# Kernel tuning notes

Measured on AMD Instinct MI355X. Metric: run time of the kernel, lower is better.

## Reference

```python
import jax, jax.numpy as jnp
import numpy as np

D_MODEL = 1024
NUM_HEADS = 16
HEAD_DIM = D_MODEL // NUM_HEADS
NEG = -1e9


def setup_inputs() -> dict:
    key = jax.random.key(0)
    kx, kq, kk, kv, ko = jax.random.split(key, 5)
    scale = 1.0 / np.sqrt(D_MODEL)
    x = jax.random.normal(kx, (4, 2048, D_MODEL), dtype=jnp.float32)
    Wq = jax.random.normal(kq, (D_MODEL, D_MODEL), dtype=jnp.float32) * scale
    Wk = jax.random.normal(kk, (D_MODEL, D_MODEL), dtype=jnp.float32) * scale
    Wv = jax.random.normal(kv, (D_MODEL, D_MODEL), dtype=jnp.float32) * scale
    Wo = jax.random.normal(ko, (D_MODEL, D_MODEL), dtype=jnp.float32) * scale
    return {"x": x, "Wq": Wq, "Wk": Wk, "Wv": Wv, "Wo": Wo}


def reference(x, Wq, Wk, Wv, Wo):
    B, S, _ = x.shape
    # torch Linear: y = x @ W.T
    q = (x @ Wq.T).reshape(B, S, NUM_HEADS, HEAD_DIM).transpose(0, 2, 1, 3)
    k = (x @ Wk.T).reshape(B, S, NUM_HEADS, HEAD_DIM).transpose(0, 2, 1, 3)
    v = (x @ Wv.T).reshape(B, S, NUM_HEADS, HEAD_DIM).transpose(0, 2, 1, 3)
    scores = jnp.einsum("bhqd,bhkd->bhqk", q, k) / jnp.sqrt(jnp.float32(HEAD_DIM))
    # additive causal mask: strictly-upper-triangular entries get -1e9 (as in source)
    mask = jnp.triu(jnp.ones((S, S), dtype=scores.dtype), k=1) * NEG
    scores = scores + mask
    attn = jax.nn.softmax(scores, axis=-1)  # dropout p=0.0 -> identity
    out = jnp.einsum("bhqk,bhkd->bhqd", attn, v)
    out = out.transpose(0, 2, 1, 3).reshape(B, S, D_MODEL)
    return out @ Wo.T
```

## Files before the change

kernel.cpp:

```cpp
#include <hip/hip_runtime.h>

typedef __attribute__((ext_vector_type(8))) short short8;
typedef __attribute__((ext_vector_type(4))) short short4v;
typedef __attribute__((ext_vector_type(4))) float f32x4;
typedef __attribute__((ext_vector_type(4))) unsigned int u32x4;

static __device__ __forceinline__ unsigned short f2bf(float f){
  unsigned u = __builtin_bit_cast(unsigned, f);
  unsigned r = u + 0x7fffu + ((u >> 16) & 1u);
  return (unsigned short)(r >> 16);
}

static __device__ __forceinline__ float exp2_fast(float x){
  float r; asm("v_exp_f32 %0, %1" : "=v"(r) : "v"(x)); return r;
}

static __device__ __forceinline__ void g2lds16(const unsigned short* g, unsigned short* l){
  __builtin_amdgcn_global_load_lds(
      (const __attribute__((address_space(1))) void*)g,
      (__attribute__((address_space(3))) void*)l, 16, 0, 0);
}

__global__ __launch_bounds__(256) void cast_bf16_kernel(const float* __restrict__ in,
                                                        unsigned short* __restrict__ out, int n8){
  int i = blockIdx.x * 256 + threadIdx.x;
  if (i >= n8) return;
  const float4* p = (const float4*)in + (size_t)i * 2;
  float4 a = p[0], b = p[1];
  short8 o;
  o[0] = (short)f2bf(a.x); o[1] = (short)f2bf(a.y); o[2] = (short)f2bf(a.z); o[3] = (short)f2bf(a.w);
  o[4] = (short)f2bf(b.x); o[5] = (short)f2bf(b.y); o[6] = (short)f2bf(b.z); o[7] = (short)f2bf(b.w);
  *(short8*)(out + (size_t)i * 8) = o;
}

__global__ __launch_bounds__(256) void cast_w4_kernel(const float* __restrict__ w0,
                                                      const float* __restrict__ w1,
                                                      const float* __restrict__ w2,
                                                      const float* __restrict__ w3,
                                                      unsigned short* __restrict__ o0,
                                                      unsigned short* __restrict__ o1,
                                                      unsigned short* __restrict__ o2,
                                                      unsigned short* __restrict__ o3){
  const int z = blockIdx.y;
  const float* in = (z == 0) ? w0 : (z == 1) ? w1 : (z == 2) ? w2 : w3;
  unsigned short* out = (z == 0) ? o0 : (z == 1) ? o1 : (z == 2) ? o2 : o3;
  int i = blockIdx.x * 256 + threadIdx.x;
  const float4* p = (const float4*)in + (size_t)i * 2;
  float4 a = p[0], b = p[1];
  short8 o;
  o[0] = (short)f2bf(a.x); o[1] = (short)f2bf(a.y); o[2] = (short)f2bf(a.z); o[3] = (short)f2bf(a.w);
  o[4] = (short)f2bf(b.x); o[5] = (short)f2bf(b.y); o[6] = (short)f2bf(b.z); o[7] = (short)f2bf(b.w);
  *(short8*)(out + (size_t)i * 8) = o;
}

template<int MODE>
__global__ __launch_bounds__(256) void gemm_nt(
    const unsigned short* __restrict__ A,
    const unsigned short* __restrict__ B0, const unsigned short* __restrict__ B1,
    const unsigned short* __restrict__ B2,
    unsigned short* __restrict__ q0, unsigned short* __restrict__ q1, unsigned short* __restrict__ q2,
    float* __restrict__ fout,
    int M, int N, int K)
{
  __shared__ unsigned short As[128 * 32];
  __shared__ unsigned short Bs[128 * 32];
  const int z = blockIdx.y;
  const unsigned short* __restrict__ B = (z == 0) ? B0 : ((z == 1) ? B1 : B2);
  unsigned short* __restrict__ qo = (z == 0) ? q0 : ((z == 1) ? q1 : q2);
  const int ntn = N >> 7;
  const int nwg = gridDim.x, cpx = nwg >> 3;
  const int bid = blockIdx.x;
  const int swz = (bid & 7) * cpx + (bid >> 3);
  const int tm = swz / ntn, tn = swz % ntn;
  const int m0 = tm << 7, n0 = tn << 7;
  const int t = threadIdx.x;
  const int w = t >> 6;
  const int l = t & 63, lo = l & 15, hi = l >> 4;
  const int wr = w >> 1, wc = w & 1;
  f32x4 acc[4][4];
#pragma unroll
  for (int i = 0; i < 4; ++i)
#pragma unroll
    for (int j = 0; j < 4; ++j) acc[i][j] = (f32x4){0.f, 0.f, 0.f, 0.f};

  const int arow0 = t >> 2, cg = t & 3;
  for (int kk = 0; kk < K; kk += 32){
#pragma unroll
    for (int r = 0; r < 2; ++r){
      int row = r * 64 + arow0;
      g2lds16(&A[(size_t)(m0 + row) * K + kk + cg * 8], &As[r * 2048 + w * 512]);
      g2lds16(&B[(size_t)(n0 + row) * K + kk + cg * 8], &Bs[r * 2048 + w * 512]);
    }
    __syncthreads();
    short8 af[4], bf[4];
#pragma unroll
    for (int mi = 0; mi < 4; ++mi) af[mi] = *(const short8*)&As[(wr * 64 + mi * 16 + lo) * 32 + hi * 8];
#pragma unroll
    for (int ni = 0; ni < 4; ++ni) bf[ni] = *(const short8*)&Bs[(wc * 64 + ni * 16 + lo) * 32 + hi * 8];
#pragma unroll
    for (int mi = 0; mi < 4; ++mi)
#pragma unroll
      for (int ni = 0; ni < 4; ++ni)
        acc[mi][ni] = __builtin_amdgcn_mfma_f32_16x16x32_bf16(af[mi], bf[ni], acc[mi][ni], 0, 0, 0);
    __syncthreads();
  }
#pragma unroll
  for (int mi = 0; mi < 4; ++mi){
#pragma unroll
    for (int ni = 0; ni < 4; ++ni){
#pragma unroll
      for (int j = 0; j < 4; ++j){
        int m = m0 + wr * 64 + mi * 16 + hi * 4 + j;
        int n = n0 + wc * 64 + ni * 16 + lo;
        float v = acc[mi][ni][j];
        if (MODE == 0){
          int b = m >> 11, s = m & 2047, h = n >> 6, d = n & 63;
          qo[((((size_t)b * 16 + h) * 2048 + s) << 6) + d] = f2bf(v);
        } else {
          fout[(size_t)m * N + n] = v;
        }
      }
    }
  }
}

__global__ __launch_bounds__(256) void transpose_v(const unsigned short* __restrict__ V,
                                                   unsigned short* __restrict__ Vt){
  __shared__ unsigned short tile[64 * 72];
  const int bh = blockIdx.y;
  const int s0 = blockIdx.x << 6;
  const int t = threadIdx.x;
  const size_t base = (size_t)bh * 2048 * 64;
#pragma unroll
  for (int r = 0; r < 2; ++r){
    int c = r * 256 + t;
    int sr = c >> 3, cgp = c & 7;
    *(short8*)&tile[sr * 72 + cgp * 8] = *(const short8*)&V[base + (size_t)(s0 + sr) * 64 + cgp * 8];
  }
  __syncthreads();
  const int d = t >> 2, sc = t & 3;
  unsigned short vals[16];
#pragma unroll
  for (int i = 0; i < 16; ++i) vals[i] = tile[(sc * 16 + i) * 72 + d];
  unsigned short* op = Vt + base + (size_t)d * 2048 + s0 + sc * 16;
  *(short8*)op = *(const short8*)&vals[0];
  *(short8*)(op + 8) = *(const short8*)&vals[8];
}

__global__ __launch_bounds__(256) void attn_kernel(
    const unsigned short* __restrict__ Q, const unsigned short* __restrict__ K,
    const unsigned short* __restrict__ Vt, unsigned short* __restrict__ O)
{
  __shared__ unsigned short Klds[2][64 * 64];
  __shared__ unsigned short Vlds[2][64 * 64];
  const int bid = blockIdx.x;
  const int xcd = bid & 7, rank = bid >> 3;
  const int bh = xcd * 8 + (rank >> 4);
  const int p = rank & 15;
  const int t = threadIdx.x, w = t >> 6, l = t & 63, lo = l & 15, hi = l >> 4;
  const size_t bb = (size_t)bh * 2048 * 64;
  const int bat = bh >> 4, h = bh & 15;
  const int srow0 = w * 8 + (l >> 3);
  const int su0 = l & 7;
  const float cexp = 0.125f * 1.44269504f;

#define STAGE(bufi, kv0) do { \
  _Pragma("unroll") \
  for (int i_ = 0; i_ < 2; ++i_){ \
    int row_ = i_ * 32 + srow0; \
    int us_ = su0 ^ (row_ & 7); \
    g2lds16(&K[bb + (size_t)((kv0) + row_) * 64 + us_ * 8], &Klds[bufi][i_ * 2048 + w * 512]); \
    g2lds16(&Vt[bb + (size_t)row_ * 2048 + (kv0) + us_ * 8], &Vlds[bufi][i_ * 2048 + w * 512]); \
  } \
} while (0)

#pragma unroll 1
  for (int ph = 0; ph < 2; ++ph){
    const int qt = ph ? (31 - p) : p;
    const int qr = qt * 64 + w * 16;
    short8 aq[2];
#pragma unroll
    for (int kg = 0; kg < 2; ++kg)
      aq[kg] = *(const short8*)&Q[bb + (size_t)(qr + lo) * 64 + kg * 32 + hi * 8];
    f32x4 accO[4];
#pragma unroll
    for (int i = 0; i < 4; ++i) accO[i] = (f32x4){0.f, 0.f, 0.f, 0.f};
    float m2 = -3e38f, lsum = 0.f;

    STAGE(0, 0);
    __syncthreads();
    int buf = 0;

#pragma unroll 1
    for (int s = 0; s <= qt; ++s){
      if (s < qt) STAGE(buf ^ 1, (s + 1) * 64);
      const unsigned short* Kl = &Klds[buf][0];
      const unsigned short* Vl = &Vlds[buf][0];
      f32x4 sa[4];
#pragma unroll
      for (int i = 0; i < 4; ++i) sa[i] = (f32x4){0.f, 0.f, 0.f, 0.f};
      __builtin_amdgcn_s_setprio(1);
#pragma unroll
      for (int ni = 0; ni < 4; ++ni)
#pragma unroll
        for (int kg = 0; kg < 2; ++kg){
          int u = (kg * 4 + hi) ^ (lo & 7);
          short8 kf = *(const short8*)&Kl[(ni * 16 + lo) * 64 + u * 8];
          sa[ni] = __builtin_amdgcn_mfma_f32_16x16x32_bf16(kf, aq[kg], sa[ni], 0, 0, 0);
        }
      __builtin_amdgcn_s_setprio(0);
      if (s == qt){
        const int qg = qr + lo;
        const int kv0 = s * 64;
#pragma unroll
        for (int ni = 0; ni < 4; ++ni)
#pragma unroll
          for (int j = 0; j < 4; ++j){
            int kv = kv0 + ni * 16 + hi * 4 + j;
            if (kv > qg) sa[ni][j] = -1e9f;
          }
      }
      float pm = fmaxf(fmaxf(sa[0][0], sa[0][1]), fmaxf(sa[0][2], sa[0][3]));
      pm = fmaxf(pm, fmaxf(fmaxf(sa[1][0], sa[1][1]), fmaxf(sa[1][2], sa[1][3])));
      pm = fmaxf(pm, fmaxf(fmaxf(sa[2][0], sa[2][1]), fmaxf(sa[2][2], sa[2][3])));
      pm = fmaxf(pm, fmaxf(fmaxf(sa[3][0], sa[3][1]), fmaxf(sa[3][2], sa[3][3])));
      float pms = pm * cexp;
      if (!__all(pms <= m2 + 8.0f)){
        float pr = fmaxf(pms, __shfl_xor(pms, 16, 64));
        pr = fmaxf(pr, __shfl_xor(pr, 32, 64));
        float m2n = fmaxf(m2, pr);
        float corr = exp2_fast(m2 - m2n);
        m2 = m2n;
        lsum *= corr;
        float cj[4];
#pragma unroll
        for (int j = 0; j < 4; ++j) cj[j] = __shfl(corr, hi * 4 + j, 64);
#pragma unroll
        for (int dt = 0; dt < 4; ++dt)
#pragma unroll
          for (int j = 0; j < 4; ++j) accO[dt][j] *= cj[j];
      }
      float rs = 0.f;
#pragma unroll
      for (int ni = 0; ni < 4; ++ni)
#pragma unroll
        for (int j = 0; j < 4; ++j){
          float pv = exp2_fast(fmaf(sa[ni][j], cexp, -m2));
          sa[ni][j] = pv;
          rs += pv;
        }
      rs += __shfl_xor(rs, 16, 64);
      rs += __shfl_xor(rs, 32, 64);
      lsum += rs;
      short8 pa[2];
#pragma unroll
      for (int kg = 0; kg < 2; ++kg){
        unsigned r0, r1, r2, r3;
        asm("v_cvt_pk_bf16_f32 %0, %1, %2" : "=v"(r0) : "v"(sa[2*kg][0]),   "v"(sa[2*kg][1]));
        asm("v_cvt_pk_bf16_f32 %0, %1, %2" : "=v"(r1) : "v"(sa[2*kg][2]),   "v"(sa[2*kg][3]));
        asm("v_cvt_pk_bf16_f32 %0, %1, %2" : "=v"(r2) : "v"(sa[2*kg+1][0]), "v"(sa[2*kg+1][1]));
        asm("v_cvt_pk_bf16_f32 %0, %1, %2" : "=v"(r3) : "v"(sa[2*kg+1][2]), "v"(sa[2*kg+1][3]));
        u32x4 pk; pk[0] = r0; pk[1] = r1; pk[2] = r2; pk[3] = r3;
        pa[kg] = __builtin_bit_cast(short8, pk);
      }
      __builtin_amdgcn_s_setprio(1);
#pragma unroll
      for (int dt = 0; dt < 4; ++dt)
#pragma unroll
        for (int kg = 0; kg < 2; ++kg){
          short4v c0, c1;
          {
            int u = ((kg * 2 + 0) * 2 + (hi >> 1)) ^ (lo & 7);
            c0 = *(const short4v*)&Vl[(dt * 16 + lo) * 64 + u * 8 + (hi & 1) * 4];
          }
          {
            int u = ((kg * 2 + 1) * 2 + (hi >> 1)) ^ (lo & 7);
            c1 = *(const short4v*)&Vl[(dt * 16 + lo) * 64 + u * 8 + (hi & 1) * 4];
          }
          short8 vb = (short8){c0[0], c0[1], c0[2], c0[3], c1[0], c1[1], c1[2], c1[3]};
          accO[dt] = __builtin_amdgcn_mfma_f32_16x16x32_bf16(pa[kg], vb, accO[dt], 0, 0, 0);
        }
      __builtin_amdgcn_s_setprio(0);
      __syncthreads();
      buf ^= 1;
    }
    float lr = 1.0f / lsum;
    float lj[4];
#pragma unroll
    for (int j = 0; j < 4; ++j) lj[j] = __shfl(lr, hi * 4 + j, 64);
#pragma unroll
    for (int dt = 0; dt < 4; ++dt)
#pragma unroll
      for (int j = 0; j < 4; ++j){
        int srow = qr + hi * 4 + j;
        O[((size_t)(bat * 2048 + srow) << 10) + h * 64 + dt * 16 + lo] = f2bf(accO[dt][j] * lj[j]);
      }
  }
#undef STAGE
}

extern "C" void kernel_launch(void* const* d_in, const int* in_sizes, int n_in,
                              void* d_out, int out_size, void* d_ws, size_t ws_size,
                              hipStream_t stream){
  (void)in_sizes; (void)n_in; (void)out_size; (void)ws_size;
  const float* x  = (const float*)d_in[0];
  const float* Wq = (const float*)d_in[1];
  const float* Wk = (const float*)d_in[2];
  const float* Wv = (const float*)d_in[3];
  const float* Wo = (const float*)d_in[4];
  char* ws = (char*)d_ws;
  const size_t MB = 1024 * 1024;
  unsigned short* XB  = (unsigned short*)(ws);
  unsigned short* WQB = (unsigned short*)(ws + 16 * MB);
  unsigned short* WKB = (unsigned short*)(ws + 18 * MB);
  unsigned short* WVB = (unsigned short*)(ws + 20 * MB);
  unsigned short* WOB = (unsigned short*)(ws + 22 * MB);
  unsigned short* Qb  = (unsigned short*)(ws + 24 * MB);
  unsigned short* Kb  = (unsigned short*)(ws + 40 * MB);
  unsigned short* Vb  = (unsigned short*)(ws + 56 * MB);
  unsigned short* Vtb = (unsigned short*)(ws + 72 * MB);
  unsigned short* Ob  = XB;

  cast_bf16_kernel<<<dim3(4096), 256, 0, stream>>>(x, XB, 8388608 / 8);
  cast_w4_kernel<<<dim3(512, 4), 256, 0, stream>>>(Wq, Wk, Wv, Wo, WQB, WKB, WVB, WOB);

  gemm_nt<0><<<dim3(512, 3), 256, 0, stream>>>(XB, WQB, WKB, WVB, Qb, Kb, Vb, nullptr,
                                               8192, 1024, 1024);
  transpose_v<<<dim3(32, 64), 256, 0, stream>>>(Vb, Vtb);
  attn_kernel<<<dim3(1024), 256, 0, stream>>>(Qb, Kb, Vtb, Ob);
  gemm_nt<1><<<dim3(512, 1), 256, 0, stream>>>(Ob, WOB, WOB, WOB, nullptr, nullptr, nullptr,
                                               (float*)d_out, 8192, 1024, 1024);
}
```

Baseline: 199.7 us.

## Split paired causal q-tiles into separate blocks and drop LDS double buffering

Each attention block now handles a single 64-row query tile instead of a balanced pair, with twice as many blocks launched and the heaviest tiles scheduled first. The K/V LDS staging is reduced to a single buffer, loaded synchronously each iteration. This halves LDS use to raise occupancy and finer-grained load balance, at the cost of losing the overlap between next-tile loads and current-tile compute.

```diff
diff --git a/kernel.cpp b/kernel.cpp
--- a/kernel.cpp
+++ b/kernel.cpp
@@ -151,12 +151,12 @@
     const unsigned short* __restrict__ Q, const unsigned short* __restrict__ K,
     const unsigned short* __restrict__ Vt, unsigned short* __restrict__ O)
 {
-  __shared__ unsigned short Klds[2][64 * 64];
-  __shared__ unsigned short Vlds[2][64 * 64];
+  __shared__ unsigned short Klds[64 * 64];
+  __shared__ unsigned short Vlds[64 * 64];
   const int bid = blockIdx.x;
   const int xcd = bid & 7, rank = bid >> 3;
-  const int bh = xcd * 8 + (rank >> 4);
-  const int p = rank & 15;
+  const int bh = xcd * 8 + (rank >> 5);
+  const int qt = 31 - (rank & 31);
   const int t = threadIdx.x, w = t >> 6, l = t & 63, lo = l & 15, hi = l >> 4;
   const size_t bb = (size_t)bh * 2048 * 64;
   const int bat = bh >> 4, h = bh & 15;
@@ -164,139 +164,126 @@
   const int su0 = l & 7;
   const float cexp = 0.125f * 1.44269504f;
 
-#define STAGE(bufi, kv0) do { \
-  _Pragma("unroll") \
-  for (int i_ = 0; i_ < 2; ++i_){ \
-    int row_ = i_ * 32 + srow0; \
-    int us_ = su0 ^ (row_ & 7); \
-    g2lds16(&K[bb + (size_t)((kv0) + row_) * 64 + us_ * 8], &Klds[bufi][i_ * 2048 + w * 512]); \
-    g2lds16(&Vt[bb + (size_t)row_ * 2048 + (kv0) + us_ * 8], &Vlds[bufi][i_ * 2048 + w * 512]); \
-  } \
-} while (0)
+  const int qr = qt * 64 + w * 16;
+  short8 aq[2];
+#pragma unroll
+  for (int kg = 0; kg < 2; ++kg)
+    aq[kg] = *(const short8*)&Q[bb + (size_t)(qr + lo) * 64 + kg * 32 + hi * 8];
+  f32x4 accO[4];
+#pragma unroll
+  for (int i = 0; i < 4; ++i) accO[i] = (f32x4){0.f, 0.f, 0.f, 0.f};
+  float m2 = -3e38f, lsum = 0.f;
 
 #pragma unroll 1
-  for (int ph = 0; ph < 2; ++ph){
-    const int qt = ph ? (31 - p) : p;
-    const int qr = qt * 64 + w * 16;
-    short8 aq[2];
-#pragma unroll
-    for (int kg = 0; kg < 2; ++kg)
-      aq[kg] = *(const short8*)&Q[bb + (size_t)(qr + lo) * 64 + kg * 32 + hi * 8];
-    f32x4 accO[4];
-#pragma unroll
-    for (int i = 0; i < 4; ++i) accO[i] = (f32x4){0.f, 0.f, 0.f, 0.f};
-    float m2 = -3e38f, lsum = 0.f;
-
-    STAGE(0, 0);
+  for (int s = 0; s <= qt; ++s){
+    const int kv0 = s * 64;
+#pragma unroll
+    for (int i_ = 0; i_ < 2; ++i_){
+      int row_ = i_ * 32 + srow0;
+      int us_ = su0 ^ (row_ & 7);
+      g2lds16(&K[bb + (size_t)(kv0 + row_) * 64 + us_ * 8], &Klds[i_ * 2048 + w * 512]);
+      g2lds16(&Vt[bb + (size_t)row_ * 2048 + kv0 + us_ * 8], &Vlds[i_ * 2048 + w * 512]);
+    }
     __syncthreads();
-    int buf = 0;
-
-#pragma unroll 1
-    for (int s = 0; s <= qt; ++s){
-      if (s < qt) STAGE(buf ^ 1, (s + 1) * 64);
-      const unsigned short* Kl = &Klds[buf][0];
-      const unsigned short* Vl = &Vlds[buf][0];
-      f32x4 sa[4];
-#pragma unroll
-      for (int i = 0; i < 4; ++i) sa[i] = (f32x4){0.f, 0.f, 0.f, 0.f};
-      __builtin_amdgcn_s_setprio(1);
+    const unsigned short* Kl = &Klds[0];
+    const unsigned short* Vl = &Vlds[0];
+    f32x4 sa[4];
+#pragma unroll
+    for (int i = 0; i < 4; ++i) sa[i] = (f32x4){0.f, 0.f, 0.f, 0.f};
+    __builtin_amdgcn_s_setprio(1);
+#pragma unroll
+    for (int ni = 0; ni < 4; ++ni)
+#pragma unroll
+      for (int kg = 0; kg < 2; ++kg){
+        int u = (kg * 4 + hi) ^ (lo & 7);
+        short8 kf = *(const short8*)&Kl[(ni * 16 + lo) * 64 + u * 8];
+        sa[ni] = __builtin_amdgcn_mfma_f32_16x16x32_bf16(kf, aq[kg], sa[ni], 0, 0, 0);
+      }
+    __builtin_amdgcn_s_setprio(0);
+    if (s == qt){
+      const int qg = qr + lo;
 #pragma unroll
       for (int ni = 0; ni < 4; ++ni)
 #pragma unroll
-        for (int kg = 0; kg < 2; ++kg){
-          int u = (kg * 4 + hi) ^ (lo & 7);
-          short8 kf = *(const short8*)&Kl[(ni * 16 + lo) * 64 + u * 8];
-          sa[ni] = __builtin_amdgcn_mfma_f32_16x16x32_bf16(kf, aq[kg], sa[ni], 0, 0, 0);
+        for (int j = 0; j < 4; ++j){
+          int kv = kv0 + ni * 16 + hi * 4 + j;
+          if (kv > qg) sa[ni][j] = -1e9f;
         }
-      __builtin_amdgcn_s_setprio(0);
-      if (s == qt){
-        const int qg = qr + lo;
-        const int kv0 = s * 64;
-#pragma unroll
-        for (int ni = 0; ni < 4; ++ni)
-#pragma unroll
-          for (int j = 0; j < 4; ++j){
-            int kv = kv0 + ni * 16 + hi * 4 + j;
-            if (kv > qg) sa[ni][j] = -1e9f;
-          }
+    }
+    float pm = fmaxf(fmaxf(sa[0][0], sa[0][1]), fmaxf(sa[0][2], sa[0][3]));
+    pm = fmaxf(pm, fmaxf(fmaxf(sa[1][0], sa[1][1]), fmaxf(sa[1][2], sa[1][3])));
+    pm = fmaxf(pm, fmaxf(fmaxf(sa[2][0], sa[2][1]), fmaxf(sa[2][2], sa[2][3])));
+    pm = fmaxf(pm, fmaxf(fmaxf(sa[3][0], sa[3][1]), fmaxf(sa[3][2], sa[3][3])));
+    float pms = pm * cexp;
+    if (!__all(pms <= m2 + 8.0f)){
+      float pr = fmaxf(pms, __shfl_xor(pms, 16, 64));
+      pr = fmaxf(pr, __shfl_xor(pr, 32, 64));
+      float m2n = fmaxf(m2, pr);
+      float corr = exp2_fast(m2 - m2n);
+      m2 = m2n;
+      lsum *= corr;
+      float cj[4];
+#pragma unroll
+      for (int j = 0; j < 4; ++j) cj[j] = __shfl(corr, hi * 4 + j, 64);
+#pragma unroll
+      for (int dt = 0; dt < 4; ++dt)
+#pragma unroll
+        for (int j = 0; j < 4; ++j) accO[dt][j] *= cj[j];
+    }
+    float rs = 0.f;
+#pragma unroll
+    for (int ni = 0; ni < 4; ++ni)
+#pragma unroll
+      for (int j = 0; j < 4; ++j){
+        float pv = exp2_fast(fmaf(sa[ni][j], cexp, -m2));
+        sa[ni][j] = pv;
+        rs += pv;
       }
-      float pm = fmaxf(fmaxf(sa[0][0], sa[0][1]), fmaxf(sa[0][2], sa[0][3]));
-      pm = fmaxf(pm, fmaxf(fmaxf(sa[1][0], sa[1][1]), fmaxf(sa[1][2], sa[1][3])));
-      pm = fmaxf(pm, fmaxf(fmaxf(sa[2][0], sa[2][1]), fmaxf(sa[2][2], sa[2][3])));
-      pm = fmaxf(pm, fmaxf(fmaxf(sa[3][0], sa[3][1]), fmaxf(sa[3][2], sa[3][3])));
-      float pms = pm * cexp;
-      if (!__all(pms <= m2 + 8.0f)){
-        float pr = fmaxf(pms, __shfl_xor(pms, 16, 64));
-        pr = fmaxf(pr, __shfl_xor(pr, 32, 64));
-        float m2n = fmaxf(m2, pr);
-        float corr = exp2_fast(m2 - m2n);
-        m2 = m2n;
-        lsum *= corr;
-        float cj[4];
-#pragma unroll
-        for (int j = 0; j < 4; ++j) cj[j] = __shfl(corr, hi * 4 + j, 64);
-#pragma unroll
-        for (int dt = 0; dt < 4; ++dt)
-#pragma unroll
-          for (int j = 0; j < 4; ++j) accO[dt][j] *= cj[j];
+    rs += __shfl_xor(rs, 16, 64);
+    rs += __shfl_xor(rs, 32, 64);
+    lsum += rs;
+    short8 pa[2];
+#pragma unroll
+    for (int kg = 0; kg < 2; ++kg){
+      unsigned r0, r1, r2, r3;
+      asm("v_cvt_pk_bf16_f32 %0, %1, %2" : "=v"(r0) : "v"(sa[2*kg][0]),   "v"(sa[2*kg][1]));
+      asm("v_cvt_pk_bf16_f32 %0, %1, %2" : "=v"(r1) : "v"(sa[2*kg][2]),   "v"(sa[2*kg][3]));
+      asm("v_cvt_pk_bf16_f32 %0, %1, %2" : "=v"(r2) : "v"(sa[2*kg+1][0]), "v"(sa[2*kg+1][1]));
+      asm("v_cvt_pk_bf16_f32 %0, %1, %2" : "=v"(r3) : "v"(sa[2*kg+1][2]), "v"(sa[2*kg+1][3]));
+      u32x4 pk; pk[0] = r0; pk[1] = r1; pk[2] = r2; pk[3] = r3;
+      pa[kg] = __builtin_bit_cast(short8, pk);
+    }
+    __builtin_amdgcn_s_setprio(1);
+#pragma unroll
+    for (int dt = 0; dt < 4; ++dt)
+#pragma unroll
+      for (int kg = 0; kg < 2; ++kg){
+        short4v c0, c1;
+        {
+          int u = ((kg * 2 + 0) * 2 + (hi >> 1)) ^ (lo & 7);
+          c0 = *(const short4v*)&Vl[(dt * 16 + lo) * 64 + u * 8 + (hi & 1) * 4];
+        }
+        {
+          int u = ((kg * 2 + 1) * 2 + (hi >> 1)) ^ (lo & 7);
+          c1 = *(const short4v*)&Vl[(dt * 16 + lo) * 64 + u * 8 + (hi & 1) * 4];
+        }
+        short8 vb = (short8){c0[0], c0[1], c0[2], c0[3], c1[0], c1[1], c1[2], c1[3]};
+        accO[dt] = __builtin_amdgcn_mfma_f32_16x16x32_bf16(pa[kg], vb, accO[dt], 0, 0, 0);
       }
-      float rs = 0.f;
-#pragma unroll
-      for (int ni = 0; ni < 4; ++ni)
-#pragma unroll
-        for (int j = 0; j < 4; ++j){
-          float pv = exp2_fast(fmaf(sa[ni][j], cexp, -m2));
-          sa[ni][j] = pv;
-          rs += pv;
-        }
-      rs += __shfl_xor(rs, 16, 64);
-      rs += __shfl_xor(rs, 32, 64);
-      lsum += rs;
-      short8 pa[2];
-#pragma unroll
-      for (int kg = 0; kg < 2; ++kg){
-        unsigned r0, r1, r2, r3;
-        asm("v_cvt_pk_bf16_f32 %0, %1, %2" : "=v"(r0) : "v"(sa[2*kg][0]),   "v"(sa[2*kg][1]));
-        asm("v_cvt_pk_bf16_f32 %0, %1, %2" : "=v"(r1) : "v"(sa[2*kg][2]),   "v"(sa[2*kg][3]));
-        asm("v_cvt_pk_bf16_f32 %0, %1, %2" : "=v"(r2) : "v"(sa[2*kg+1][0]), "v"(sa[2*kg+1][1]));
-        asm("v_cvt_pk_bf16_f32 %0, %1, %2" : "=v"(r3) : "v"(sa[2*kg+1][2]), "v"(sa[2*kg+1][3]));
-        u32x4 pk; pk[0] = r0; pk[1] = r1; pk[2] = r2; pk[3] = r3;
-        pa[kg] = __builtin_bit_cast(short8, pk);
-      }
-      __builtin_amdgcn_s_setprio(1);
-#pragma unroll
-      for (int dt = 0; dt < 4; ++dt)
-#pragma unroll
-        for (int kg = 0; kg < 2; ++kg){
-          short4v c0, c1;
-          {
-            int u = ((kg * 2 + 0) * 2 + (hi >> 1)) ^ (lo & 7);
-            c0 = *(const short4v*)&Vl[(dt * 16 + lo) * 64 + u * 8 + (hi & 1) * 4];
-          }
-          {
-            int u = ((kg * 2 + 1) * 2 + (hi >> 1)) ^ (lo & 7);
-            c1 = *(const short4v*)&Vl[(dt * 16 + lo) * 64 + u * 8 + (hi & 1) * 4];
-          }
-          short8 vb = (short8){c0[0], c0[1], c0[2], c0[3], c1[0], c1[1], c1[2], c1[3]};
-          accO[dt] = __builtin_amdgcn_mfma_f32_16x16x32_bf16(pa[kg], vb, accO[dt], 0, 0, 0);
-        }
-      __builtin_amdgcn_s_setprio(0);
-      __syncthreads();
-      buf ^= 1;
-    }
-    float lr = 1.0f / lsum;
-    float lj[4];
-#pragma unroll
-    for (int j = 0; j < 4; ++j) lj[j] = __shfl(lr, hi * 4 + j, 64);
-#pragma unroll
-    for (int dt = 0; dt < 4; ++dt)
-#pragma unroll
-      for (int j = 0; j < 4; ++j){
-        int srow = qr + hi * 4 + j;
-        O[((size_t)(bat * 2048 + srow) << 10) + h * 64 + dt * 16 + lo] = f2bf(accO[dt][j] * lj[j]);
-      }
+    __builtin_amdgcn_s_setprio(0);
+    __syncthreads();
   }
-#undef STAGE
+  float lr = 1.0f / lsum;
+  float lj[4];
+#pragma unroll
+  for (int j = 0; j < 4; ++j) lj[j] = __shfl(lr, hi * 4 + j, 64);
+#pragma unroll
+  for (int dt = 0; dt < 4; ++dt)
+#pragma unroll
+    for (int j = 0; j < 4; ++j){
+      int srow = qr + hi * 4 + j;
+      O[((size_t)(bat * 2048 + srow) << 10) + h * 64 + dt * 16 + lo] = f2bf(accO[dt][j] * lj[j]);
+    }
 }
 
 extern "C" void kernel_launch(void* const* d_in, const int* in_sizes, int n_in,
@@ -327,7 +314,7 @@
   gemm_nt<0><<<dim3(512, 3), 256, 0, stream>>>(XB, WQB, WKB, WVB, Qb, Kb, Vb, nullptr,
                                                8192, 1024, 1024);
   transpose_v<<<dim3(32, 64), 256, 0, stream>>>(Vb, Vtb);
-  attn_kernel<<<dim3(1024), 256, 0, stream>>>(Qb, Kb, Vtb, Ob);
+  attn_kernel<<<dim3(2048), 256, 0, stream>>>(Qb, Kb, Vtb, Ob);
   gemm_nt<1><<<dim3(512, 1), 256, 0, stream>>>(Ob, WOB, WOB, WOB, nullptr, nullptr, nullptr,
                                                (float*)d_out, 8192, 1024, 1024);
 }
```

Measured after the change: 220.2 us. 1.1x slower.

## Double-buffer GEMM LDS loads with 256x128 tiles and 512-thread blocks

Applied to the files above, without the earlier changes.

Rewrites the bf16 NT GEMM to use 512 threads (8 waves) on a 256x128 output tile with K-step 64. LDS is double-buffered so the global-to-LDS copy of the next K tile overlaps the MFMA work on the current one. Waits use explicit vmcnt counts, and s_setprio is raised around the MFMA bursts. The projection and output GEMM grids are halved to match, and the larger tile and LDS footprint (96KB) lower the number of resident blocks per CU.

```diff
diff --git a/kernel.cpp b/kernel.cpp
--- a/kernel.cpp
+++ b/kernel.cpp
@@ -54,7 +54,7 @@
 }
 
 template<int MODE>
-__global__ __launch_bounds__(256) void gemm_nt(
+__global__ __launch_bounds__(512) void gemm_nt(
     const unsigned short* __restrict__ A,
     const unsigned short* __restrict__ B0, const unsigned short* __restrict__ B1,
     const unsigned short* __restrict__ B2,
@@ -62,8 +62,8 @@
     float* __restrict__ fout,
     int M, int N, int K)
 {
-  __shared__ unsigned short As[128 * 32];
-  __shared__ unsigned short Bs[128 * 32];
+  __shared__ __attribute__((aligned(16))) unsigned short Abuf[32768];
+  __shared__ __attribute__((aligned(16))) unsigned short Bbuf[16384];
   const int z = blockIdx.y;
   const unsigned short* __restrict__ B = (z == 0) ? B0 : ((z == 1) ? B1 : B2);
   unsigned short* __restrict__ qo = (z == 0) ? q0 : ((z == 1) ? q1 : q2);
@@ -72,47 +72,94 @@
   const int bid = blockIdx.x;
   const int swz = (bid & 7) * cpx + (bid >> 3);
   const int tm = swz / ntn, tn = swz % ntn;
-  const int m0 = tm << 7, n0 = tn << 7;
+  const int m0 = tm << 8, n0 = tn << 7;
   const int t = threadIdx.x;
-  const int w = t >> 6;
-  const int l = t & 63, lo = l & 15, hi = l >> 4;
+  const int w = t >> 6, l = t & 63, lo = l & 15, hi = l >> 4;
   const int wr = w >> 1, wc = w & 1;
+  const int arow = l >> 2, kc = (l & 3) << 3;
+
+  const unsigned short* gA0 = A + (size_t)(m0 + (w * 2 + 0) * 16 + arow) * K + kc;
+  const unsigned short* gA1 = A + (size_t)(m0 + (w * 2 + 1) * 16 + arow) * K + kc;
+  const unsigned short* gB  = B + (size_t)(n0 + w * 16 + arow) * K + kc;
+
   f32x4 acc[4][4];
 #pragma unroll
   for (int i = 0; i < 4; ++i)
 #pragma unroll
     for (int j = 0; j < 4; ++j) acc[i][j] = (f32x4){0.f, 0.f, 0.f, 0.f};
 
-  const int arow0 = t >> 2, cg = t & 3;
-  for (int kk = 0; kk < K; kk += 32){
-#pragma unroll
-    for (int r = 0; r < 2; ++r){
-      int row = r * 64 + arow0;
-      g2lds16(&A[(size_t)(m0 + row) * K + kk + cg * 8], &As[r * 2048 + w * 512]);
-      g2lds16(&B[(size_t)(n0 + row) * K + kk + cg * 8], &Bs[r * 2048 + w * 512]);
-    }
-    __syncthreads();
-    short8 af[4], bf[4];
-#pragma unroll
-    for (int mi = 0; mi < 4; ++mi) af[mi] = *(const short8*)&As[(wr * 64 + mi * 16 + lo) * 32 + hi * 8];
-#pragma unroll
-    for (int ni = 0; ni < 4; ++ni) bf[ni] = *(const short8*)&Bs[(wc * 64 + ni * 16 + lo) * 32 + hi * 8];
-#pragma unroll
-    for (int mi = 0; mi < 4; ++mi)
-#pragma unroll
-      for (int ni = 0; ni < 4; ++ni)
-        acc[mi][ni] = __builtin_amdgcn_mfma_f32_16x16x32_bf16(af[mi], bf[ni], acc[mi][ni], 0, 0, 0);
-    __syncthreads();
+#define STG(bufi, kt, kh) do { \
+    g2lds16(gA0 + (kt) * 64 + (kh) * 32, &Abuf[(bufi) * 16384 + (kh) * 8192 + (w * 2 + 0) * 512]); \
+    g2lds16(gA1 + (kt) * 64 + (kh) * 32, &Abuf[(bufi) * 16384 + (kh) * 8192 + (w * 2 + 1) * 512]); \
+    g2lds16(gB  + (kt) * 64 + (kh) * 32, &Bbuf[(bufi) * 8192  + (kh) * 4096 + w * 512]); \
+  } while (0)
+
+  STG(0, 0, 0);
+  STG(0, 0, 1);
+
+  const int KT = K >> 6;
+#pragma unroll 1
+  for (int kt = 0; kt < KT; ++kt){
+    const int buf = kt & 1;
+    const unsigned short* Ab = &Abuf[buf * 16384];
+    const unsigned short* Bb = &Bbuf[buf * 8192];
+    const bool more = (kt + 1 < KT);
+    asm volatile("s_waitcnt vmcnt(3)" ::: "memory");
+    __builtin_amdgcn_s_barrier();
+    __builtin_amdgcn_sched_barrier(0);
+    if (more) STG(buf ^ 1, kt + 1, 0);
+    {
+      short8 af[4], bf[4];
+#pragma unroll
+      for (int mf = 0; mf < 4; ++mf)
+        af[mf] = *(const short8*)&Ab[(wr * 64 + mf * 16 + lo) * 32 + hi * 8];
+#pragma unroll
+      for (int nf = 0; nf < 4; ++nf)
+        bf[nf] = *(const short8*)&Bb[(wc * 64 + nf * 16 + lo) * 32 + hi * 8];
+      __builtin_amdgcn_s_setprio(1);
+#pragma unroll
+      for (int mf = 0; mf < 4; ++mf)
+#pragma unroll
+        for (int nf = 0; nf < 4; ++nf)
+          acc[mf][nf] = __builtin_amdgcn_mfma_f32_16x16x32_bf16(af[mf], bf[nf], acc[mf][nf], 0, 0, 0);
+      __builtin_amdgcn_s_setprio(0);
+    }
+    if (more){
+      asm volatile("s_waitcnt vmcnt(3)" ::: "memory");
+    } else {
+      asm volatile("s_waitcnt vmcnt(0)" ::: "memory");
+    }
+    __builtin_amdgcn_s_barrier();
+    __builtin_amdgcn_sched_barrier(0);
+    if (more) STG(buf ^ 1, kt + 1, 1);
+    {
+      short8 af[4], bf[4];
+#pragma unroll
+      for (int mf = 0; mf < 4; ++mf)
+        af[mf] = *(const short8*)&Ab[8192 + (wr * 64 + mf * 16 + lo) * 32 + hi * 8];
+#pragma unroll
+      for (int nf = 0; nf < 4; ++nf)
+        bf[nf] = *(const short8*)&Bb[4096 + (wc * 64 + nf * 16 + lo) * 32 + hi * 8];
+      __builtin_amdgcn_s_setprio(1);
+#pragma unroll
+      for (int mf = 0; mf < 4; ++mf)
+#pragma unroll
+        for (int nf = 0; nf < 4; ++nf)
+          acc[mf][nf] = __builtin_amdgcn_mfma_f32_16x16x32_bf16(af[mf], bf[nf], acc[mf][nf], 0, 0, 0);
+      __builtin_amdgcn_s_setprio(0);
+    }
   }
-#pragma unroll
-  for (int mi = 0; mi < 4; ++mi){
-#pragma unroll
-    for (int ni = 0; ni < 4; ++ni){
+#undef STG
+
+#pragma unroll
+  for (int mf = 0; mf < 4; ++mf){
+#pragma unroll
+    for (int nf = 0; nf < 4; ++nf){
 #pragma unroll
       for (int j = 0; j < 4; ++j){
-        int m = m0 + wr * 64 + mi * 16 + hi * 4 + j;
-        int n = n0 + wc * 64 + ni * 16 + lo;
-        float v = acc[mi][ni][j];
+        int m = m0 + wr * 64 + mf * 16 + hi * 4 + j;
+        int n = n0 + wc * 64 + nf * 16 + lo;
+        float v = acc[mf][nf][j];
         if (MODE == 0){
           int b = m >> 11, s = m & 2047, h = n >> 6, d = n & 63;
           qo[((((size_t)b * 16 + h) * 2048 + s) << 6) + d] = f2bf(v);
@@ -324,10 +371,10 @@
   cast_bf16_kernel<<<dim3(4096), 256, 0, stream>>>(x, XB, 8388608 / 8);
   cast_w4_kernel<<<dim3(512, 4), 256, 0, stream>>>(Wq, Wk, Wv, Wo, WQB, WKB, WVB, WOB);
 
-  gemm_nt<0><<<dim3(512, 3), 256, 0, stream>>>(XB, WQB, WKB, WVB, Qb, Kb, Vb, nullptr,
+  gemm_nt<0><<<dim3(256, 3), 512, 0, stream>>>(XB, WQB, WKB, WVB, Qb, Kb, Vb, nullptr,
                                                8192, 1024, 1024);
   transpose_v<<<dim3(32, 64), 256, 0, stream>>>(Vb, Vtb);
   attn_kernel<<<dim3(1024), 256, 0, stream>>>(Qb, Kb, Vtb, Ob);
-  gemm_nt<1><<<dim3(512, 1), 256, 0, stream>>>(Ob, WOB, WOB, WOB, nullptr, nullptr, nullptr,
+  gemm_nt<1><<<dim3(256, 1), 512, 0, stream>>>(Ob, WOB, WOB, WOB, nullptr, nullptr, nullptr,
                                                (float*)d_out, 8192, 1024, 1024);
 }
```

Result: slower. 218.2 us (+9.2%).

## Double GEMM K-tile to 64 with XOR-swizzled LDS layout and MFMA priority

Applied to the files above, without the earlier changes.

The NT GEMM used for the QKV and output projections now stages a K depth of 64 per iteration instead of 32, which halves the number of barrier pairs per tile. Each 16-byte chunk is stored at an XOR-swizzled column within its LDS row, and the fragment reads apply the same swizzle, to avoid bank conflicts on the wider 128-byte rows. MFMA sections are wrapped in s_setprio to favour the compute waves. LDS use doubles to 32KB per block, which may reduce occupancy.

```diff
diff --git a/kernel.cpp b/kernel.cpp
--- a/kernel.cpp
+++ b/kernel.cpp
@@ -62,8 +62,8 @@
     float* __restrict__ fout,
     int M, int N, int K)
 {
-  __shared__ unsigned short As[128 * 32];
-  __shared__ unsigned short Bs[128 * 32];
+  __shared__ __attribute__((aligned(16))) unsigned short As[128 * 64];
+  __shared__ __attribute__((aligned(16))) unsigned short Bs[128 * 64];
   const int z = blockIdx.y;
   const unsigned short* __restrict__ B = (z == 0) ? B0 : ((z == 1) ? B1 : B2);
   unsigned short* __restrict__ qo = (z == 0) ? q0 : ((z == 1) ? q1 : q2);
@@ -83,36 +83,51 @@
 #pragma unroll
     for (int j = 0; j < 4; ++j) acc[i][j] = (f32x4){0.f, 0.f, 0.f, 0.f};
 
-  const int arow0 = t >> 2, cg = t & 3;
-  for (int kk = 0; kk < K; kk += 32){
-#pragma unroll
-    for (int r = 0; r < 2; ++r){
-      int row = r * 64 + arow0;
-      g2lds16(&A[(size_t)(m0 + row) * K + kk + cg * 8], &As[r * 2048 + w * 512]);
-      g2lds16(&B[(size_t)(n0 + row) * K + kk + cg * 8], &Bs[r * 2048 + w * 512]);
+  const int srow = t >> 3;
+  const int us = (l & 7) ^ (srow & 7);
+  const unsigned short* gA = A + (size_t)(m0 + srow) * K + us * 8;
+  const unsigned short* gB = B + (size_t)(n0 + srow) * K + us * 8;
+
+  const int u0 = (((0 * 4 + hi) ^ (lo & 7)) * 8);
+  const int u1 = (((1 * 4 + hi) ^ (lo & 7)) * 8);
+
+  for (int kk = 0; kk < K; kk += 64){
+#pragma unroll
+    for (int i = 0; i < 4; ++i){
+      g2lds16(gA + (size_t)(i * 32) * K + kk, &As[i * 2048 + w * 512]);
+      g2lds16(gB + (size_t)(i * 32) * K + kk, &Bs[i * 2048 + w * 512]);
     }
     __syncthreads();
-    short8 af[4], bf[4];
-#pragma unroll
-    for (int mi = 0; mi < 4; ++mi) af[mi] = *(const short8*)&As[(wr * 64 + mi * 16 + lo) * 32 + hi * 8];
-#pragma unroll
-    for (int ni = 0; ni < 4; ++ni) bf[ni] = *(const short8*)&Bs[(wc * 64 + ni * 16 + lo) * 32 + hi * 8];
-#pragma unroll
-    for (int mi = 0; mi < 4; ++mi)
-#pragma unroll
-      for (int ni = 0; ni < 4; ++ni)
-        acc[mi][ni] = __builtin_amdgcn_mfma_f32_16x16x32_bf16(af[mi], bf[ni], acc[mi][ni], 0, 0, 0);
+#pragma unroll
+    for (int kh = 0; kh < 2; ++kh){
+      const int uu = kh ? u1 : u0;
+      short8 af[4], bf[4];
+#pragma unroll
+      for (int mf = 0; mf < 4; ++mf)
+        af[mf] = *(const short8*)&As[(wr * 64 + mf * 16 + lo) * 64 + uu];
+#pragma unroll
+      for (int nf = 0; nf < 4; ++nf)
+        bf[nf] = *(const short8*)&Bs[(wc * 64 + nf * 16 + lo) * 64 + uu];
+      __builtin_amdgcn_s_setprio(1);
+#pragma unroll
+      for (int mf = 0; mf < 4; ++mf)
+#pragma unroll
+        for (int nf = 0; nf < 4; ++nf)
+          acc[mf][nf] = __builtin_amdgcn_mfma_f32_16x16x32_bf16(af[mf], bf[nf], acc[mf][nf], 0, 0, 0);
+      __builtin_amdgcn_s_setprio(0);
+    }
     __syncthreads();
   }
-#pragma unroll
-  for (int mi = 0; mi < 4; ++mi){
-#pragma unroll
-    for (int ni = 0; ni < 4; ++ni){
+
+#pragma unroll
+  for (int mf = 0; mf < 4; ++mf){
+#pragma unroll
+    for (int nf = 0; nf < 4; ++nf){
 #pragma unroll
       for (int j = 0; j < 4; ++j){
-        int m = m0 + wr * 64 + mi * 16 + hi * 4 + j;
-        int n = n0 + wc * 64 + ni * 16 + lo;
-        float v = acc[mi][ni][j];
+        int m = m0 + wr * 64 + mf * 16 + hi * 4 + j;
+        int n = n0 + wc * 64 + nf * 16 + lo;
+        float v = acc[mf][nf][j];
         if (MODE == 0){
           int b = m >> 11, s = m & 2047, h = n >> 6, d = n & 63;
           qo[((((size_t)b * 16 + h) * 2048 + s) << 6) + d] = f2bf(v);
```

New measurement: 179.2 us. 1.11x faster.
